# Kernel tuning notes

Hardware: AMD Instinct MI355X
Metric: run time of the kernel (lower is better)

The kernel has to match this reference:

```python
import jax, jax.numpy as jnp
import numpy as np

B, T = 128, 2048
O, E, L = 128, 512, 34  # o_size, embed_dim, num_letter


def setup_inputs() -> dict:
    key = jax.random.key(0)
    ks = jax.random.split(key, 16)
    u = lambda k, shape, s: jax.random.uniform(k, shape, jnp.float32, -s, s)
    hk = jax.random.normal(ks[0], (B, T, O), jnp.float32)
    hv = jax.random.normal(ks[1], (B, T, O), jnp.float32)
    y_1 = jax.random.normal(ks[2], (B, E), jnp.float32)
    c_1 = jax.random.normal(ks[3], (B, O), jnp.float32)
    sh_1 = jax.random.normal(ks[4], (B, O), jnp.float32)
    sc_1 = jax.random.normal(ks[5], (B, O), jnp.float32)
    # valid-length mask (each row has at least T//2 valid positions)
    lengths = jax.random.randint(ks[6], (B,), T // 2, T + 1)
    mask = (jnp.arange(T)[None, :] < lengths[:, None]).astype(jnp.float32)
    s_rnn = 1.0 / np.sqrt(O)
    W_ih = u(ks[7], (4 * O, O + E), s_rnn)
    b_ih = u(ks[8], (4 * O,), s_rnn)
    W_hh = u(ks[9], (4 * O, O), s_rnn)
    b_hh = u(ks[10], (4 * O,), s_rnn)
    s1 = 1.0 / np.sqrt(O)
    W1 = u(ks[11], (L, O), s1); b1 = u(ks[12], (L,), s1)
    W2 = u(ks[13], (L, O), s1); b2 = u(ks[14], (L,), s1)
    s3 = 1.0 / np.sqrt(L)
    W3 = u(ks[15], (L, L), s3); b3 = u(jax.random.fold_in(key, 99), (L,), s3)
    return {"hk": hk, "hv": hv, "y_1": y_1, "c_1": c_1, "sh_1": sh_1,
            "sc_1": sc_1, "mask": mask, "W_ih": W_ih, "b_ih": b_ih,
            "W_hh": W_hh, "b_hh": b_hh, "W1": W1, "b1": b1,
            "W2": W2, "b2": b2, "W3": W3, "b3": b3}


def reference(hk, hv, y_1, c_1, sh_1, sc_1, mask,
              W_ih, b_ih, W_hh, b_hh, W1, b1, W2, b2, W3, b3):
    # LSTMCell (PyTorch gate order: i, f, g, o)
    x = jnp.concatenate([y_1, c_1], axis=1)            # [B, O+E]
    gates = x @ W_ih.T + b_ih + sh_1 @ W_hh.T + b_hh   # [B, 4O]
    i, f, g, o = jnp.split(gates, 4, axis=1)
    sc = jax.nn.sigmoid(f) * sc_1 + jax.nn.sigmoid(i) * jnp.tanh(g)
    sh = jax.nn.sigmoid(o) * jnp.tanh(sc)
    # attention scores keyed on cell state sc (faithful to source)
    scores = jnp.einsum('bto,bo->bt', hk, sc)          # [B, T]
    attn = jax.nn.softmax(scores, axis=1) * mask
    attn = attn / jnp.sum(attn, axis=1, keepdims=True)
    c = jnp.einsum('bt,bto->bo', attn, hv)             # [B, O]
    out = jax.nn.relu(sh @ W1.T + b1 + c @ W2.T + b2)
    out = jax.nn.softmax(out @ W3.T + b3, axis=1)      # [B, L]
    return (out, c, sh, sc)
```

## Files before the change

### kernel.cpp

```cpp
#include <hip/hip_runtime.h>
#include <math.h>

#define BB 128
#define TT 2048
#define OO 128
#define EE 512
#define LL 34
#define XDIM 640
#define CHUNKS 16
#define CHUNK_LEN 128

__device__ __forceinline__ float sigmoidf_(float x) { return 1.0f / (1.0f + __expf(-x)); }

__global__ __launch_bounds__(256) void lstm_kernel(
    const float* __restrict__ y1, const float* __restrict__ c1,
    const float* __restrict__ sh1, const float* __restrict__ sc1,
    const float* __restrict__ Wih, const float* __restrict__ bih,
    const float* __restrict__ Whh, const float* __restrict__ bhh,
    float* __restrict__ out_sh, float* __restrict__ out_sc)
{
    __shared__ float xs[4][768];
    __shared__ float gbuf[4][4][16];
    const int tid = threadIdx.x;
    const int otile = blockIdx.x;
    const int qb = blockIdx.y * 4;

    for (int idx = tid; idx < 4 * 768; idx += 256) {
        int bi = idx / 768, k = idx - bi * 768;
        int b = qb + bi;
        float v;
        if (k < 512)      v = y1[b * EE + k];
        else if (k < 640) v = c1[b * OO + (k - 512)];
        else              v = sh1[b * OO + (k - 640)];
        xs[bi][k] = v;
    }
    __syncthreads();

    const int g = tid >> 6, l = tid & 63;
    #pragma unroll 2
    for (int i = 0; i < 16; ++i) {
        const int row = g * 128 + otile * 16 + i;
        const float* wr = Wih + (size_t)row * XDIM;
        float a0 = 0.f, a1 = 0.f, a2 = 0.f, a3 = 0.f;
        #pragma unroll
        for (int j = 0; j < 10; ++j) {
            float wv = wr[l + 64 * j];
            a0 += wv * xs[0][l + 64 * j];
            a1 += wv * xs[1][l + 64 * j];
            a2 += wv * xs[2][l + 64 * j];
            a3 += wv * xs[3][l + 64 * j];
        }
        const float* wh = Whh + (size_t)row * OO;
        #pragma unroll
        for (int j = 0; j < 2; ++j) {
            float wv = wh[l + 64 * j];
            a0 += wv * xs[0][640 + l + 64 * j];
            a1 += wv * xs[1][640 + l + 64 * j];
            a2 += wv * xs[2][640 + l + 64 * j];
            a3 += wv * xs[3][640 + l + 64 * j];
        }
        #pragma unroll
        for (int off = 32; off >= 1; off >>= 1) {
            a0 += __shfl_xor(a0, off);
            a1 += __shfl_xor(a1, off);
            a2 += __shfl_xor(a2, off);
            a3 += __shfl_xor(a3, off);
        }
        if (l == 0) {
            float bb = bih[row] + bhh[row];
            gbuf[g][0][i] = a0 + bb;
            gbuf[g][1][i] = a1 + bb;
            gbuf[g][2][i] = a2 + bb;
            gbuf[g][3][i] = a3 + bb;
        }
    }
    __syncthreads();

    if (tid < 64) {
        const int bi = tid >> 4, ol = tid & 15;
        const int b = qb + bi, o = otile * 16 + ol;
        float gi = gbuf[0][bi][ol], gf = gbuf[1][bi][ol];
        float gg = gbuf[2][bi][ol], go = gbuf[3][bi][ol];
        float sc = sigmoidf_(gf) * sc1[b * OO + o] + sigmoidf_(gi) * tanhf(gg);
        float sh = sigmoidf_(go) * tanhf(sc);
        out_sc[b * OO + o] = sc;
        out_sh[b * OO + o] = sh;
    }
}

__global__ __launch_bounds__(256) void scores_kernel(
    const float* __restrict__ hk, const float* __restrict__ mask,
    const float* __restrict__ sc, float* __restrict__ wbuf,
    float2* __restrict__ pbuf)
{
    const int b = blockIdx.y, chunk = blockIdx.x;
    const int tid = threadIdx.x;
    const int sg = tid >> 4, l = tid & 15;

    const float4 scA = *(const float4*)(sc + b * OO + l * 8);
    const float4 scB = *(const float4*)(sc + b * OO + l * 8 + 4);

    const int r0 = chunk * CHUNK_LEN + sg * 8;
    const float* mrow = mask + (size_t)b * TT + r0;
    const float* krow = hk + ((size_t)b * TT + r0) * OO;

    float s[8];
    bool val[8];
    #pragma unroll
    for (int i = 0; i < 8; ++i) {
        val[i] = (mrow[i] != 0.f);
        float4 a = make_float4(0.f, 0.f, 0.f, 0.f);
        float4 c2 = make_float4(0.f, 0.f, 0.f, 0.f);
        if (val[i]) {
            a  = *(const float4*)(krow + (size_t)i * OO + l * 8);
            c2 = *(const float4*)(krow + (size_t)i * OO + l * 8 + 4);
        }
        s[i] = a.x * scA.x + a.y * scA.y + a.z * scA.z + a.w * scA.w
             + c2.x * scB.x + c2.y * scB.y + c2.z * scB.z + c2.w * scB.w;
    }
    #pragma unroll
    for (int i = 0; i < 8; ++i) {
        s[i] += __shfl_xor(s[i], 8);
        s[i] += __shfl_xor(s[i], 4);
        s[i] += __shfl_xor(s[i], 2);
        s[i] += __shfl_xor(s[i], 1);
    }
    float msg = -INFINITY;
    #pragma unroll
    for (int i = 0; i < 8; ++i) if (val[i]) msg = fmaxf(msg, s[i]);

    __shared__ float sm[16], ssum[16];
    if (l == 0) sm[sg] = msg;
    __syncthreads();
    float mc = sm[0];
    #pragma unroll
    for (int i = 1; i < 16; ++i) mc = fmaxf(mc, sm[i]);

    float psum = 0.f;
    float e[8];
    #pragma unroll
    for (int i = 0; i < 8; ++i) {
        e[i] = val[i] ? __expf(s[i] - mc) : 0.f;
        psum += e[i];
    }
    if (l == 0) ssum[sg] = psum;
    float* wrow = wbuf + (size_t)b * TT + r0;
    #pragma unroll
    for (int i = 0; i < 8; ++i)
        if (l == i) wrow[i] = e[i];
    __syncthreads();
    if (tid == 0) {
        float S = 0.f;
        #pragma unroll
        for (int i = 0; i < 16; ++i) S += ssum[i];
        pbuf[(size_t)b * CHUNKS + chunk] = make_float2(mc, S);
    }
}

__global__ __launch_bounds__(256) void wsum_kernel(
    const float* __restrict__ hv, const float* __restrict__ wbuf,
    const float2* __restrict__ pbuf, float* __restrict__ ws_c)
{
    const int b = blockIdx.y, chunk = blockIdx.x;
    const int tid = threadIdx.x;
    __shared__ float marr[CHUNKS], Sarr[CHUNKS];
    __shared__ float wsh[CHUNK_LEN];
    __shared__ float pacc[8][128];

    if (tid < CHUNKS) {
        float2 p = pbuf[(size_t)b * CHUNKS + tid];
        marr[tid] = p.x;
        Sarr[tid] = p.y;
    }
    __syncthreads();
    float M = marr[0];
    #pragma unroll
    for (int i = 1; i < CHUNKS; ++i) M = fmaxf(M, marr[i]);
    float S = 0.f;
    #pragma unroll
    for (int i = 0; i < CHUNKS; ++i) S += Sarr[i] * __expf(marr[i] - M);
    const float factor = __expf(marr[chunk] - M) / S;

    if (tid < CHUNK_LEN)
        wsh[tid] = wbuf[(size_t)b * TT + chunk * CHUNK_LEN + tid] * factor;
    __syncthreads();

    const int o4 = tid & 31, rr = tid >> 5;
    const float* vbase = hv + ((size_t)b * TT + chunk * CHUNK_LEN) * OO + o4 * 4;
    float4 acc = make_float4(0.f, 0.f, 0.f, 0.f);
    #pragma unroll 8
    for (int j = 0; j < 16; ++j) {
        const int r = rr + 8 * j;
        const float wr = wsh[r];
        if (wr != 0.f) {
            float4 v = *(const float4*)(vbase + (size_t)r * OO);
            acc.x += wr * v.x;
            acc.y += wr * v.y;
            acc.z += wr * v.z;
            acc.w += wr * v.w;
        }
    }
    *(float4*)&pacc[rr][o4 * 4] = acc;
    __syncthreads();

    if (tid < 128) {
        float s = 0.f;
        #pragma unroll
        for (int i = 0; i < 8; ++i) s += pacc[i][tid];
        ws_c[((size_t)b * CHUNKS + chunk) * OO + tid] = s;
    }
}

__global__ __launch_bounds__(256) void final_kernel(
    const float* __restrict__ ws_c, const float* __restrict__ sh_in,
    const float* __restrict__ W1, const float* __restrict__ b1,
    const float* __restrict__ W2, const float* __restrict__ b2,
    const float* __restrict__ W3, const float* __restrict__ b3,
    float* __restrict__ out_p, float* __restrict__ out_c)
{
    const int b = blockIdx.x, tid = threadIdx.x;
    __shared__ float cbuf[128], shbuf[128], h1[LL], zz[LL], red2[2];

    if (tid < 128) {
        float s = 0.f;
        const float* base = ws_c + (size_t)b * CHUNKS * OO + tid;
        #pragma unroll
        for (int i = 0; i < CHUNKS; ++i) s += base[i * OO];
        cbuf[tid] = s;
        out_c[b * OO + tid] = s;
        shbuf[tid] = sh_in[b * OO + tid];
    }
    __syncthreads();

    const int o = tid >> 2, l2 = tid & 3;
    if (o < LL) {
        float a = 0.f;
        const float* w1r = W1 + o * OO;
        const float* w2r = W2 + o * OO;
        #pragma unroll 8
        for (int j = 0; j < 32; ++j) {
            int k = l2 + 4 * j;
            a += w1r[k] * shbuf[k] + w2r[k] * cbuf[k];
        }
        a += __shfl_xor(a, 1);
        a += __shfl_xor(a, 2);
        if (l2 == 0) h1[o] = fmaxf(a + b1[o] + b2[o], 0.f);
    }
    __syncthreads();

    if (o < LL) {
        float z = 0.f;
        const float* w3r = W3 + o * LL;
        for (int j = 0; j < 9; ++j) {
            int k = l2 + 4 * j;
            if (k < LL) z += w3r[k] * h1[k];
        }
        z += __shfl_xor(z, 1);
        z += __shfl_xor(z, 2);
        if (l2 == 0) zz[o] = z + b3[o];
    }
    __syncthreads();
    if (tid == 0) {
        float mm = zz[0];
        for (int i = 1; i < LL; i++) mm = fmaxf(mm, zz[i]);
        float ss = 0.f;
        for (int i = 0; i < LL; i++) ss += __expf(zz[i] - mm);
        red2[0] = mm; red2[1] = ss;
    }
    __syncthreads();
    if (tid < LL) out_p[b * LL + tid] = __expf(zz[tid] - red2[0]) / red2[1];
}

extern "C" void kernel_launch(void* const* d_in, const int* in_sizes, int n_in,
                              void* d_out, int out_size, void* d_ws, size_t ws_size,
                              hipStream_t stream) {
    (void)in_sizes; (void)n_in; (void)out_size; (void)ws_size;
    const float* hk   = (const float*)d_in[0];
    const float* hv   = (const float*)d_in[1];
    const float* y1   = (const float*)d_in[2];
    const float* c1   = (const float*)d_in[3];
    const float* sh1  = (const float*)d_in[4];
    const float* sc1  = (const float*)d_in[5];
    const float* mask = (const float*)d_in[6];
    const float* Wih  = (const float*)d_in[7];
    const float* bih  = (const float*)d_in[8];
    const float* Whh  = (const float*)d_in[9];
    const float* bhh  = (const float*)d_in[10];
    const float* W1   = (const float*)d_in[11];
    const float* b1   = (const float*)d_in[12];
    const float* W2   = (const float*)d_in[13];
    const float* b2   = (const float*)d_in[14];
    const float* W3   = (const float*)d_in[15];
    const float* b3   = (const float*)d_in[16];

    float* out    = (float*)d_out;
    float* out_c  = out + BB * LL;
    float* out_sh = out_c + BB * OO;
    float* out_sc = out_sh + BB * OO;

    float*  wbuf = (float*)d_ws;
    float*  ws_c = wbuf + (size_t)BB * TT;
    float2* pbuf = (float2*)(ws_c + (size_t)BB * CHUNKS * OO);

    lstm_kernel<<<dim3(8, 32), 256, 0, stream>>>(y1, c1, sh1, sc1, Wih, bih, Whh, bhh,
                                                 out_sh, out_sc);
    scores_kernel<<<dim3(CHUNKS, BB), 256, 0, stream>>>(hk, mask, out_sc, wbuf, pbuf);
    wsum_kernel<<<dim3(CHUNKS, BB), 256, 0, stream>>>(hv, wbuf, pbuf, ws_c);
    final_kernel<<<BB, 256, 0, stream>>>(ws_c, out_sh, W1, b1, W2, b2, W3, b3,
                                         out, out_c);
}
```

Before: 326.0 us.

## Fuse scores and weighted-sum into one flash-style attention kernel

Merges the scores and weighted-sum kernels into one attention kernel. Each chunk now produces unnormalized partial context vectors plus its (max, sum) pair, and the final kernel rescales and combines the chunks. hv loads are issued early into registers so they overlap the hk dot products and reductions. This removes one launch, the wbuf round trip, and the dependency between the two passes, at the cost of higher register pressure from 16 float4 buffers per thread.

```diff
diff --git a/kernel.cpp b/kernel.cpp
--- a/kernel.cpp
+++ b/kernel.cpp
@@ -88,14 +88,19 @@
     }
 }
 
-__global__ __launch_bounds__(256) void scores_kernel(
-    const float* __restrict__ hk, const float* __restrict__ mask,
-    const float* __restrict__ sc, float* __restrict__ wbuf,
-    float2* __restrict__ pbuf)
+__global__ __launch_bounds__(256) void attn_kernel(
+    const float* __restrict__ hk, const float* __restrict__ hv,
+    const float* __restrict__ mask, const float* __restrict__ sc,
+    float* __restrict__ ws_c, float2* __restrict__ pbuf)
 {
     const int b = blockIdx.y, chunk = blockIdx.x;
     const int tid = threadIdx.x;
     const int sg = tid >> 4, l = tid & 15;
+    const int o4 = tid & 31, rr = tid >> 5;
+
+    __shared__ float sm[16], ssum[16];
+    __shared__ float wsh[CHUNK_LEN];
+    __shared__ float pacc[8][128];
 
     const float4 scA = *(const float4*)(sc + b * OO + l * 8);
     const float4 scB = *(const float4*)(sc + b * OO + l * 8 + 4);
@@ -104,12 +109,14 @@
     const float* mrow = mask + (size_t)b * TT + r0;
     const float* krow = hk + ((size_t)b * TT + r0) * OO;
 
+    bool val[8];
+    #pragma unroll
+    for (int i = 0; i < 8; ++i) val[i] = (mrow[i] != 0.f);
+
     float s[8];
-    bool val[8];
     #pragma unroll
     for (int i = 0; i < 8; ++i) {
-        val[i] = (mrow[i] != 0.f);
-        float4 a = make_float4(0.f, 0.f, 0.f, 0.f);
+        float4 a  = make_float4(0.f, 0.f, 0.f, 0.f);
         float4 c2 = make_float4(0.f, 0.f, 0.f, 0.f);
         if (val[i]) {
             a  = *(const float4*)(krow + (size_t)i * OO + l * 8);
@@ -118,6 +125,18 @@
         s[i] = a.x * scA.x + a.y * scA.y + a.z * scA.z + a.w * scA.w
              + c2.x * scB.x + c2.y * scB.y + c2.z * scB.z + c2.w * scB.w;
     }
+
+    const float* mrowB = mask + (size_t)b * TT + chunk * CHUNK_LEN;
+    const float* vbase = hv + ((size_t)b * TT + chunk * CHUNK_LEN) * OO + o4 * 4;
+    float4 hvb[16];
+    #pragma unroll
+    for (int j = 0; j < 16; ++j) {
+        const int r = rr + 8 * j;
+        hvb[j] = make_float4(0.f, 0.f, 0.f, 0.f);
+        if (mrowB[r] != 0.f)
+            hvb[j] = *(const float4*)(vbase + (size_t)r * OO);
+    }
+
     #pragma unroll
     for (int i = 0; i < 8; ++i) {
         s[i] += __shfl_xor(s[i], 8);
@@ -129,7 +148,6 @@
     #pragma unroll
     for (int i = 0; i < 8; ++i) if (val[i]) msg = fmaxf(msg, s[i]);
 
-    __shared__ float sm[16], ssum[16];
     if (l == 0) sm[sg] = msg;
     __syncthreads();
     float mc = sm[0];
@@ -143,89 +161,73 @@
         e[i] = val[i] ? __expf(s[i] - mc) : 0.f;
         psum += e[i];
     }
+    #pragma unroll
+    for (int i = 0; i < 8; ++i)
+        if (l == i) wsh[sg * 8 + i] = e[i];
     if (l == 0) ssum[sg] = psum;
-    float* wrow = wbuf + (size_t)b * TT + r0;
-    #pragma unroll
-    for (int i = 0; i < 8; ++i)
-        if (l == i) wrow[i] = e[i];
-    __syncthreads();
+    __syncthreads();
+
     if (tid == 0) {
         float S = 0.f;
         #pragma unroll
         for (int i = 0; i < 16; ++i) S += ssum[i];
         pbuf[(size_t)b * CHUNKS + chunk] = make_float2(mc, S);
     }
+
+    float4 acc = make_float4(0.f, 0.f, 0.f, 0.f);
+    #pragma unroll
+    for (int j = 0; j < 16; ++j) {
+        const float w = wsh[rr + 8 * j];
+        acc.x += w * hvb[j].x;
+        acc.y += w * hvb[j].y;
+        acc.z += w * hvb[j].z;
+        acc.w += w * hvb[j].w;
+    }
+    *(float4*)&pacc[rr][o4 * 4] = acc;
+    __syncthreads();
+
+    if (tid < 128) {
+        float t = 0.f;
+        #pragma unroll
+        for (int i = 0; i < 8; ++i) t += pacc[i][tid];
+        ws_c[((size_t)b * CHUNKS + chunk) * OO + tid] = t;
+    }
 }
 
-__global__ __launch_bounds__(256) void wsum_kernel(
-    const float* __restrict__ hv, const float* __restrict__ wbuf,
-    const float2* __restrict__ pbuf, float* __restrict__ ws_c)
-{
-    const int b = blockIdx.y, chunk = blockIdx.x;
-    const int tid = threadIdx.x;
-    __shared__ float marr[CHUNKS], Sarr[CHUNKS];
-    __shared__ float wsh[CHUNK_LEN];
-    __shared__ float pacc[8][128];
-
-    if (tid < CHUNKS) {
-        float2 p = pbuf[(size_t)b * CHUNKS + tid];
-        marr[tid] = p.x;
-        Sarr[tid] = p.y;
-    }
-    __syncthreads();
-    float M = marr[0];
-    #pragma unroll
-    for (int i = 1; i < CHUNKS; ++i) M = fmaxf(M, marr[i]);
-    float S = 0.f;
-    #pragma unroll
-    for (int i = 0; i < CHUNKS; ++i) S += Sarr[i] * __expf(marr[i] - M);
-    const float factor = __expf(marr[chunk] - M) / S;
-
-    if (tid < CHUNK_LEN)
-        wsh[tid] = wbuf[(size_t)b * TT + chunk * CHUNK_LEN + tid] * factor;
-    __syncthreads();
-
-    const int o4 = tid & 31, rr = tid >> 5;
-    const float* vbase = hv + ((size_t)b * TT + chunk * CHUNK_LEN) * OO + o4 * 4;
-    float4 acc = make_float4(0.f, 0.f, 0.f, 0.f);
-    #pragma unroll 8
-    for (int j = 0; j < 16; ++j) {
-        const int r = rr + 8 * j;
-        const float wr = wsh[r];
-        if (wr != 0.f) {
-            float4 v = *(const float4*)(vbase + (size_t)r * OO);
-            acc.x += wr * v.x;
-            acc.y += wr * v.y;
-            acc.z += wr * v.z;
-            acc.w += wr * v.w;
-        }
-    }
-    *(float4*)&pacc[rr][o4 * 4] = acc;
-    __syncthreads();
-
-    if (tid < 128) {
-        float s = 0.f;
-        #pragma unroll
-        for (int i = 0; i < 8; ++i) s += pacc[i][tid];
-        ws_c[((size_t)b * CHUNKS + chunk) * OO + tid] = s;
-    }
-}
-
 __global__ __launch_bounds__(256) void final_kernel(
-    const float* __restrict__ ws_c, const float* __restrict__ sh_in,
+    const float* __restrict__ ws_c, const float2* __restrict__ pbuf,
+    const float* __restrict__ sh_in,
     const float* __restrict__ W1, const float* __restrict__ b1,
     const float* __restrict__ W2, const float* __restrict__ b2,
     const float* __restrict__ W3, const float* __restrict__ b3,
     float* __restrict__ out_p, float* __restrict__ out_c)
 {
     const int b = blockIdx.x, tid = threadIdx.x;
+    __shared__ float marr[CHUNKS], Sarr[CHUNKS], fac[CHUNKS];
     __shared__ float cbuf[128], shbuf[128], h1[LL], zz[LL], red2[2];
+
+    if (tid < CHUNKS) {
+        float2 p = pbuf[(size_t)b * CHUNKS + tid];
+        marr[tid] = p.x;
+        Sarr[tid] = p.y;
+    }
+    __syncthreads();
+    if (tid < CHUNKS) {
+        float M = marr[0];
+        #pragma unroll
+        for (int i = 1; i < CHUNKS; ++i) M = fmaxf(M, marr[i]);
+        float S = 0.f;
+        #pragma unroll
+        for (int i = 0; i < CHUNKS; ++i) S += Sarr[i] * __expf(marr[i] - M);
+        fac[tid] = __expf(marr[tid] - M) / S;
+    }
+    __syncthreads();
 
     if (tid < 128) {
         float s = 0.f;
         const float* base = ws_c + (size_t)b * CHUNKS * OO + tid;
         #pragma unroll
-        for (int i = 0; i < CHUNKS; ++i) s += base[i * OO];
+        for (int i = 0; i < CHUNKS; ++i) s += fac[i] * base[i * OO];
         cbuf[tid] = s;
         out_c[b * OO + tid] = s;
         shbuf[tid] = sh_in[b * OO + tid];
@@ -298,14 +300,12 @@
     float* out_sh = out_c + BB * OO;
     float* out_sc = out_sh + BB * OO;
 
-    float*  wbuf = (float*)d_ws;
-    float*  ws_c = wbuf + (size_t)BB * TT;
+    float*  ws_c = (float*)d_ws;
     float2* pbuf = (float2*)(ws_c + (size_t)BB * CHUNKS * OO);
 
     lstm_kernel<<<dim3(8, 32), 256, 0, stream>>>(y1, c1, sh1, sc1, Wih, bih, Whh, bhh,
                                                  out_sh, out_sc);
-    scores_kernel<<<dim3(CHUNKS, BB), 256, 0, stream>>>(hk, mask, out_sc, wbuf, pbuf);
-    wsum_kernel<<<dim3(CHUNKS, BB), 256, 0, stream>>>(hv, wbuf, pbuf, ws_c);
-    final_kernel<<<BB, 256, 0, stream>>>(ws_c, out_sh, W1, b1, W2, b2, W3, b3,
+    attn_kernel<<<dim3(CHUNKS, BB), 256, 0, stream>>>(hk, hv, mask, out_sc, ws_c, pbuf);
+    final_kernel<<<BB, 256, 0, stream>>>(ws_c, pbuf, out_sh, W1, b1, W2, b2, W3, b3,
                                          out, out_c);
 }
```

Result: no change. 327.1 us (+0.3%).
